# Optimization experiments

Measured on AMD Instinct MI355X. Metric: run time of the kernel, lower is better.

Reference implementation:

```python
import jax, jax.numpy as jnp
import numpy as np

NUM_SAMPLE = 10


def setup_inputs() -> dict:
    key = jax.random.key(0)
    k1, k2, k3, k4, k5 = jax.random.split(key, 5)
    N, F, B, S = 100000, 256, 20000, NUM_SAMPLE
    features_ue = jax.random.normal(k1, (N, F), dtype=jnp.float32)
    features_ap = jax.random.normal(k2, (N, F), dtype=jnp.float32)
    neigh_idx = jax.random.randint(k3, (B, S), 0, N, dtype=jnp.int32)
    nodes = jax.random.randint(k4, (B,), 0, N, dtype=jnp.int32)
    # xavier-uniform weight [embed_dim, feature_dim] = [256, 2*F]
    embed_dim, feature_dim = 256, 2 * F
    limit = float(np.sqrt(6.0 / (embed_dim + feature_dim)))
    weight = jax.random.uniform(k5, (embed_dim, feature_dim), dtype=jnp.float32,
                                minval=-limit, maxval=limit)
    return {"features_ue": features_ue, "features_ap": features_ap,
            "neigh_idx": neigh_idx, "nodes": nodes, "weight": weight}


def reference(features_ue, features_ap, neigh_idx, nodes, weight):
    # sample_model='ue2ue': other_feature = self_feature = features_ue
    S = neigh_idx.shape[1]
    # gather sampled neighbor features: [B, S, F] -> sum over S
    gathered = jnp.take(features_ue, neigh_idx, axis=0)
    # original: mask.div(num_neigh + 1), i.e. divide by count PLUS one
    neigh_feats = gathered.sum(axis=1) / jnp.float32(S + 1)  # [B, F]
    self_feats = jnp.take(features_ue, nodes, axis=0)        # [B, F]
    combined = jnp.concatenate([self_feats, neigh_feats], axis=1)  # [B, 2F]
    # weight.mm(combined.t()) then relu -> [embed_dim, B]
    out = jax.nn.relu(jnp.einsum('ef,bf->eb', weight, combined))
    return out
```

## Files before the change

kernel.cpp:

```cpp
#include <hip/hip_runtime.h>

typedef __attribute__((ext_vector_type(8))) short short8;
typedef __attribute__((ext_vector_type(4))) float f32x4;

#define B_TOTAL 20000
#define B_PAD   20096
#define NF      256
#define K2      512
#define NS      10

__device__ __forceinline__ unsigned short f2bf(float x) {
    unsigned u = __builtin_bit_cast(unsigned, x);
    u += 0x7FFFu + ((u >> 16) & 1u);
    return (unsigned short)(u >> 16);
}

__global__ __launch_bounds__(256) void gather_combine(
    const float* __restrict__ ue, const int* __restrict__ nidx,
    const int* __restrict__ nodes, const float* __restrict__ w,
    unsigned short* __restrict__ comb, unsigned short* __restrict__ wbf)
{
    const int t = threadIdx.x, blk = blockIdx.x;
    if (blk < 128) {
        const int base = blk * 1024 + t * 4;
        const float4 v = *(const float4*)(w + base);
        ushort4 o;
        o.x = f2bf(v.x); o.y = f2bf(v.y); o.z = f2bf(v.z); o.w = f2bf(v.w);
        *(ushort4*)(wbf + base) = o;
    }
    const int lane = t & 63;
    const int b = blk * 4 + (t >> 6);
    if (b >= B_PAD) return;
    unsigned short* crow = comb + (size_t)b * K2;
    if (b < B_TOTAL) {
        const int node = nodes[b];
        const float4 sf = ((const float4*)(ue + (size_t)node * NF))[lane];
        int myidx = 0;
        if (lane < NS) myidx = nidx[b * NS + lane];
        float ax = 0.f, ay = 0.f, az = 0.f, aw = 0.f;
        #pragma unroll
        for (int s = 0; s < NS; ++s) {
            const int is = __shfl(myidx, s);
            const float4 v = ((const float4*)(ue + (size_t)is * NF))[lane];
            ax += v.x; ay += v.y; az += v.z; aw += v.w;
        }
        const float inv = 1.0f / 11.0f;
        ushort4 s4, n4;
        s4.x = f2bf(sf.x); s4.y = f2bf(sf.y); s4.z = f2bf(sf.z); s4.w = f2bf(sf.w);
        n4.x = f2bf(ax * inv); n4.y = f2bf(ay * inv);
        n4.z = f2bf(az * inv); n4.w = f2bf(aw * inv);
        *(ushort4*)(crow + lane * 4) = s4;
        *(ushort4*)(crow + NF + lane * 4) = n4;
    } else {
        ushort4 z; z.x = z.y = z.z = z.w = 0;
        *(ushort4*)(crow + lane * 4) = z;
        *(ushort4*)(crow + NF + lane * 4) = z;
    }
}

__global__ __launch_bounds__(256) void gemm_relu(
    const unsigned short* __restrict__ wbf,
    const unsigned short* __restrict__ comb,
    float* __restrict__ out)
{
    __shared__ unsigned short Alds[2][4096];
    __shared__ unsigned short Blds[2][2048];
    const int t    = threadIdx.x;
    const int lane = t & 63;
    const int wv   = t >> 6;
    const int n0   = blockIdx.x * 64;
    const int m0   = blockIdx.y * 128;
    const int fr   = lane & 15;
    const int kq   = lane >> 4;

    const int arow = t & 127, akg = t >> 7;
    const int brow = t & 63,  bkg = t >> 6;

    const unsigned short* gaBase = wbf  + (size_t)(m0 + arow) * K2 + akg * 8;
    const unsigned short* gbBase = comb + (size_t)(n0 + brow) * K2 + bkg * 8;

#define STAGE(nb, ks)                                                            \
    do {                                                                         \
        const unsigned short* ga = gaBase + (ks) * 32;                           \
        const unsigned short* gb = gbBase + (ks) * 32;                           \
        __builtin_amdgcn_global_load_lds(                                        \
            (const __attribute__((address_space(1))) void*)ga,                   \
            (__attribute__((address_space(3))) void*)(&Alds[nb][0] + t * 8),     \
            16, 0, 0);                                                           \
        __builtin_amdgcn_global_load_lds(                                        \
            (const __attribute__((address_space(1))) void*)(ga + 16),            \
            (__attribute__((address_space(3))) void*)(&Alds[nb][2048] + t * 8),  \
            16, 0, 0);                                                           \
        __builtin_amdgcn_global_load_lds(                                        \
            (const __attribute__((address_space(1))) void*)gb,                   \
            (__attribute__((address_space(3))) void*)(&Blds[nb][0] + t * 8),     \
            16, 0, 0);                                                           \
    } while (0)

    f32x4 acc[2][4] = {};

    STAGE(0, 0);
    __syncthreads();

    #pragma unroll
    for (int ks = 0; ks < 16; ++ks) {
        const int cur = ks & 1;
        if (ks < 15) STAGE(cur ^ 1, ks + 1);

        const short8* A8 = (const short8*)Alds[cur];
        const short8* B8 = (const short8*)Blds[cur];
        short8 af[2], bg[4];
        #pragma unroll
        for (int i = 0; i < 2; ++i)
            af[i] = A8[kq * 128 + wv * 32 + i * 16 + fr];
        #pragma unroll
        for (int j = 0; j < 4; ++j)
            bg[j] = B8[kq * 64 + j * 16 + fr];
        #pragma unroll
        for (int i = 0; i < 2; ++i)
            #pragma unroll
            for (int j = 0; j < 4; ++j)
                acc[i][j] = __builtin_amdgcn_mfma_f32_16x16x32_bf16(af[i], bg[j], acc[i][j], 0, 0, 0);

        __syncthreads();
    }
#undef STAGE

    #pragma unroll
    for (int i = 0; i < 2; ++i) {
        const int e = m0 + wv * 32 + i * 16 + kq * 4;
        #pragma unroll
        for (int j = 0; j < 4; ++j) {
            const int b = n0 + j * 16 + fr;
            if (b < B_TOTAL) {
                #pragma unroll
                for (int r = 0; r < 4; ++r)
                    out[(size_t)(e + r) * B_TOTAL + b] = fmaxf(acc[i][j][r], 0.0f);
            }
        }
    }
}

extern "C" void kernel_launch(void* const* d_in, const int* in_sizes, int n_in,
                              void* d_out, int out_size, void* d_ws, size_t ws_size,
                              hipStream_t stream) {
    const float* ue    = (const float*)d_in[0];
    const int*   nidx  = (const int*)d_in[2];
    const int*   nodes = (const int*)d_in[3];
    const float* w     = (const float*)d_in[4];
    float*       out   = (float*)d_out;

    unsigned short* comb = (unsigned short*)d_ws;
    unsigned short* wbf  = comb + (size_t)B_PAD * K2;

    hipLaunchKernelGGL(gather_combine, dim3(B_PAD / 4), dim3(256), 0, stream,
                       ue, nidx, nodes, w, comb, wbf);
    hipLaunchKernelGGL(gemm_relu, dim3(B_PAD / 64, 2), dim3(256), 0, stream,
                       wbf, comb, out);
}
```

Before: 61.55 us.

## Double K-tile depth in GEMM and use explicit vmcnt waits for prefetch

New measurement: 62.92 us. +2.2%, slower.

```diff
diff --git a/kernel.cpp b/kernel.cpp
--- a/kernel.cpp
+++ b/kernel.cpp
@@ -63,8 +63,8 @@
     const unsigned short* __restrict__ comb,
     float* __restrict__ out)
 {
-    __shared__ unsigned short Alds[2][4096];
-    __shared__ unsigned short Blds[2][2048];
+    __shared__ unsigned short Alds[2][8192];
+    __shared__ unsigned short Blds[2][4096];
     const int t    = threadIdx.x;
     const int lane = t & 63;
     const int wv   = t >> 6;
@@ -73,58 +73,72 @@
     const int fr   = lane & 15;
     const int kq   = lane >> 4;
 
-    const int arow = t & 127, akg = t >> 7;
-    const int brow = t & 63,  bkg = t >> 6;
+#define STAGE(buf, ks)                                                           \
+    do {                                                                         \
+        _Pragma("unroll")                                                        \
+        for (int L = 0; L < 4; ++L) {                                            \
+            const int d = L * 256 + t;                                           \
+            const unsigned short* src =                                          \
+                wbf + (size_t)(m0 + (d & 127)) * K2 + (ks) * 64 + (d >> 7) * 8;  \
+            __builtin_amdgcn_global_load_lds(                                    \
+                (const __attribute__((address_space(1))) void*)src,              \
+                (__attribute__((address_space(3))) void*)(&Alds[buf][0] + d * 8),\
+                16, 0, 0);                                                       \
+        }                                                                        \
+        _Pragma("unroll")                                                        \
+        for (int L = 0; L < 2; ++L) {                                            \
+            const int d = L * 256 + t;                                           \
+            const unsigned short* src =                                          \
+                comb + (size_t)(n0 + (d & 63)) * K2 + (ks) * 64 + (d >> 6) * 8;  \
+            __builtin_amdgcn_global_load_lds(                                    \
+                (const __attribute__((address_space(1))) void*)src,              \
+                (__attribute__((address_space(3))) void*)(&Blds[buf][0] + d * 8),\
+                16, 0, 0);                                                       \
+        }                                                                        \
+    } while (0)
 
-    const unsigned short* gaBase = wbf  + (size_t)(m0 + arow) * K2 + akg * 8;
-    const unsigned short* gbBase = comb + (size_t)(n0 + brow) * K2 + bkg * 8;
-
-#define STAGE(nb, ks)                                                            \
+#define COMPUTE(buf)                                                             \
     do {                                                                         \
-        const unsigned short* ga = gaBase + (ks) * 32;                           \
-        const unsigned short* gb = gbBase + (ks) * 32;                           \
-        __builtin_amdgcn_global_load_lds(                                        \
-            (const __attribute__((address_space(1))) void*)ga,                   \
-            (__attribute__((address_space(3))) void*)(&Alds[nb][0] + t * 8),     \
-            16, 0, 0);                                                           \
-        __builtin_amdgcn_global_load_lds(                                        \
-            (const __attribute__((address_space(1))) void*)(ga + 16),            \
-            (__attribute__((address_space(3))) void*)(&Alds[nb][2048] + t * 8),  \
-            16, 0, 0);                                                           \
-        __builtin_amdgcn_global_load_lds(                                        \
-            (const __attribute__((address_space(1))) void*)gb,                   \
-            (__attribute__((address_space(3))) void*)(&Blds[nb][0] + t * 8),     \
-            16, 0, 0);                                                           \
+        const short8* A8 = (const short8*)Alds[buf];                             \
+        const short8* B8 = (const short8*)Blds[buf];                             \
+        _Pragma("unroll")                                                        \
+        for (int h = 0; h < 2; ++h) {                                            \
+            short8 af[2], bg[4];                                                 \
+            _Pragma("unroll")                                                    \
+            for (int i = 0; i < 2; ++i)                                          \
+                af[i] = A8[(h * 4 + kq) * 128 + wv * 32 + i * 16 + fr];          \
+            _Pragma("unroll")                                                    \
+            for (int j = 0; j < 4; ++j)                                          \
+                bg[j] = B8[(h * 4 + kq) * 64 + j * 16 + fr];                     \
+            _Pragma("unroll")                                                    \
+            for (int i = 0; i < 2; ++i)                                          \
+                _Pragma("unroll")                                                \
+                for (int j = 0; j < 4; ++j)                                      \
+                    acc[i][j] = __builtin_amdgcn_mfma_f32_16x16x32_bf16(         \
+                        af[i], bg[j], acc[i][j], 0, 0, 0);                       \
+        }                                                                        \
     } while (0)
 
     f32x4 acc[2][4] = {};
 
     STAGE(0, 0);
-    __syncthreads();
-
     #pragma unroll
-    for (int ks = 0; ks < 16; ++ks) {
-        const int cur = ks & 1;
-        if (ks < 15) STAGE(cur ^ 1, ks + 1);
-
-        const short8* A8 = (const short8*)Alds[cur];
-        const short8* B8 = (const short8*)Blds[cur];
-        short8 af[2], bg[4];
-        #pragma unroll
-        for (int i = 0; i < 2; ++i)
-            af[i] = A8[kq * 128 + wv * 32 + i * 16 + fr];
-        #pragma unroll
-        for (int j = 0; j < 4; ++j)
-            bg[j] = B8[kq * 64 + j * 16 + fr];
-        #pragma unroll
-        for (int i = 0; i < 2; ++i)
-            #pragma unroll
-            for (int j = 0; j < 4; ++j)
-                acc[i][j] = __builtin_amdgcn_mfma_f32_16x16x32_bf16(af[i], bg[j], acc[i][j], 0, 0, 0);
-
-        __syncthreads();
+    for (int it = 0; it < 8; ++it) {
+        const int c = it & 1;
+        if (it < 7) {
+            if (c == 0) STAGE(1, it + 1); else STAGE(0, it + 1);
+            asm volatile("s_waitcnt vmcnt(6)" ::: "memory");
+        } else {
+            asm volatile("s_waitcnt vmcnt(0)" ::: "memory");
+        }
+        __builtin_amdgcn_s_barrier();
+        __builtin_amdgcn_sched_barrier(0);
+        if (c == 0) COMPUTE(0); else COMPUTE(1);
+        __builtin_amdgcn_sched_barrier(0);
+        __builtin_amdgcn_s_barrier();
     }
 #undef STAGE
+#undef COMPUTE
 
     #pragma unroll
     for (int i = 0; i < 2; ++i) {
```
